# Kernel optimization log

Hardware: AMD Instinct MI355X
Metric: run time of the kernel (lower is better)

## Reference

```python
import jax, jax.numpy as jnp
import numpy as np


def fwht(x):
    """Unnormalized Fast Walsh-Hadamard transform along axis 0 (Sylvester order).
    Equivalent to H @ x where H is the +/-1 Hadamard matrix. x.shape[0] must be a power of 2."""
    D = x.shape[0]
    orig_shape = x.shape
    x = x.reshape(D, -1)
    h = 1
    while h < D:
        x = x.reshape(D // (2 * h), 2, h, -1)
        a = x[:, 0]
        b = x[:, 1]
        x = jnp.stack([a + b, a - b], axis=1)
        h *= 2
    return x.reshape(orig_shape)


def setup_inputs() -> dict:
    D = 4096
    B = 2048
    key = jax.random.key(0)
    k_x, k_eps, k_rho = jax.random.split(key, 3)
    x = jax.random.normal(k_x, (B, D), dtype=jnp.float32)
    epsilon = jax.random.normal(k_eps, (D,), dtype=jnp.float32)
    s1 = jnp.ones((D,), dtype=jnp.float32) * 0.01
    s2 = jnp.ones((D,), dtype=jnp.float32) * 0.01
    g_mu = jnp.zeros((D,), dtype=jnp.float32)
    # g_rho ~ Uniform(-5, -4) as in the torch init
    g_rho = jax.random.uniform(k_rho, (D,), dtype=jnp.float32, minval=-5.0, maxval=-4.0)
    return {"x": x, "epsilon": epsilon, "s1": s1, "s2": s2, "g_mu": g_mu, "g_rho": g_rho}


def reference(x, epsilon, s1, s2, g_mu, g_rho):
    D = s1.shape[0]
    # g_sigma_sqrt_diagonal = softplus(g_rho); sampled diag g = g_mu + sigma * eps.
    # W = diag(s1) @ H @ diag(g) @ H @ diag(s2); mu and sigma terms are linear in g, so combine.
    g = g_mu + jax.nn.softplus(g_rho) * epsilon
    # HS2 = H * s2 (columns of H scaled by s2) = H @ diag(s2) = fwht(diag(s2)) along axis 0
    HS2 = fwht(jnp.diag(s2))                      # [D, D]
    W = s1[:, None] * fwht(g[:, None] * HS2)      # [D, D]
    # F.linear(x, W) = x @ W^T
    return x @ W.T
```

## Files before the change

### kernel.cpp

```cpp
#include <hip/hip_runtime.h>
#include <math.h>

#define DIM 4096
#define ROWS 2048

__global__ void g_precompute(const float* __restrict__ eps,
                             const float* __restrict__ g_mu,
                             const float* __restrict__ g_rho,
                             float* __restrict__ g, int n) {
    int i = blockIdx.x * blockDim.x + threadIdx.x;
    if (i < n) {
        float sp = log1pf(expf(g_rho[i]));
        g[i] = g_mu[i] + sp * eps[i];
    }
}

__device__ __forceinline__ float4 f4mul(float4 a, float4 b) {
    return make_float4(a.x * b.x, a.y * b.y, a.z * b.z, a.w * b.w);
}

__device__ __forceinline__ void lane_stage(float4 v[16], int m, float sg) {
#pragma unroll
    for (int j = 0; j < 16; ++j) {
        float px = __shfl_xor(v[j].x, m, 64);
        float py = __shfl_xor(v[j].y, m, 64);
        float pz = __shfl_xor(v[j].z, m, 64);
        float pw = __shfl_xor(v[j].w, m, 64);
        v[j].x = fmaf(sg, v[j].x, px);
        v[j].y = fmaf(sg, v[j].y, py);
        v[j].z = fmaf(sg, v[j].z, pz);
        v[j].w = fmaf(sg, v[j].w, pw);
    }
}

__device__ __forceinline__ void fwht4096(float4 v[16], const float sg[6]) {
#pragma unroll
    for (int j = 0; j < 16; ++j) {
        float4 a = v[j];
        float t0 = a.x + a.y, t1 = a.x - a.y;
        float t2 = a.z + a.w, t3 = a.z - a.w;
        v[j] = make_float4(t0 + t2, t1 + t3, t0 - t2, t1 - t3);
    }
#pragma unroll
    for (int s = 0; s < 6; ++s)
        lane_stage(v, 1 << s, sg[s]);
#pragma unroll
    for (int m = 1; m < 16; m <<= 1) {
#pragma unroll
        for (int j = 0; j < 16; ++j) {
            if (!(j & m)) {
                int k = j | m;
                float4 a = v[j], b = v[k];
                v[j] = make_float4(a.x + b.x, a.y + b.y, a.z + b.z, a.w + b.w);
                v[k] = make_float4(a.x - b.x, a.y - b.y, a.z - b.z, a.w - b.w);
            }
        }
    }
}

__global__ void __launch_bounds__(256, 2)
whvi_main(const float* __restrict__ x, const float* __restrict__ s1,
          const float* __restrict__ s2, const float* __restrict__ g,
          float* __restrict__ out) {
    const int lane = threadIdx.x & 63;
    const int row  = blockIdx.x * 4 + (threadIdx.x >> 6);
    if (row >= ROWS) return;

    const float4* __restrict__ xr  = (const float4*)(x + (size_t)row * DIM);
    float4* __restrict__       orw = (float4*)(out + (size_t)row * DIM);
    const float4* __restrict__ s2v = (const float4*)s2;
    const float4* __restrict__ gv  = (const float4*)g;
    const float4* __restrict__ s1v = (const float4*)s1;

    float sg[6];
#pragma unroll
    for (int s = 0; s < 6; ++s)
        sg[s] = (lane & (1 << s)) ? -1.0f : 1.0f;

    float4 v[16];
#pragma unroll
    for (int j = 0; j < 16; ++j)
        v[j] = f4mul(xr[lane + 64 * j], s2v[lane + 64 * j]);

    fwht4096(v, sg);

#pragma unroll
    for (int j = 0; j < 16; ++j)
        v[j] = f4mul(v[j], gv[lane + 64 * j]);

    fwht4096(v, sg);

#pragma unroll
    for (int j = 0; j < 16; ++j)
        orw[lane + 64 * j] = f4mul(v[j], s1v[lane + 64 * j]);
}

extern "C" void kernel_launch(void* const* d_in, const int* in_sizes, int n_in,
                              void* d_out, int out_size, void* d_ws, size_t ws_size,
                              hipStream_t stream) {
    const float* x     = (const float*)d_in[0];
    const float* eps   = (const float*)d_in[1];
    const float* s1    = (const float*)d_in[2];
    const float* s2    = (const float*)d_in[3];
    const float* g_mu  = (const float*)d_in[4];
    const float* g_rho = (const float*)d_in[5];
    float* out = (float*)d_out;
    float* g   = (float*)d_ws;

    g_precompute<<<DIM / 256, 256, 0, stream>>>(eps, g_mu, g_rho, g, DIM);
    whvi_main<<<ROWS / 4, 256, 0, stream>>>(x, s1, s2, g, out);
}
```

Measured before the change: 107.0 us.

## Replace cross-lane shuffle FWHT stages with LDS transpose and in-register butterflies

Replaces the six __shfl_xor butterfly stages of each 4096-point FWHT with a padded LDS transpose, so the lane-dimension stages run as in-register butterflies on 64 values per thread. The two middle FWHT passes are merged around the g scaling, which needs only two transposes, and g is precomputed in a permuted layout to match. This cuts shuffle traffic (12 stages × 64 shuffles per thread) but adds LDS use of about 66KB per block and a 64-float register array, which may lower occupancy or cause spills. The launch-bounds minimum-blocks hint is dropped.

```diff
diff --git a/kernel.cpp b/kernel.cpp
--- a/kernel.cpp
+++ b/kernel.cpp
@@ -3,37 +3,24 @@
 
 #define DIM 4096
 #define ROWS 2048
+#define LSTR 65
 
 __global__ void g_precompute(const float* __restrict__ eps,
                              const float* __restrict__ g_mu,
                              const float* __restrict__ g_rho,
-                             float* __restrict__ g, int n) {
-    int i = blockIdx.x * blockDim.x + threadIdx.x;
-    if (i < n) {
-        float sp = log1pf(expf(g_rho[i]));
-        g[i] = g_mu[i] + sp * eps[i];
-    }
+                             float* __restrict__ g_t) {
+    int t = blockIdx.x * blockDim.x + threadIdx.x;
+    int lp = t >> 6, m = t & 63;
+    int j = 256 * (lp >> 2) + 4 * m + (lp & 3);
+    float sp = log1pf(expf(g_rho[j]));
+    g_t[t] = g_mu[j] + sp * eps[j];
 }
 
 __device__ __forceinline__ float4 f4mul(float4 a, float4 b) {
     return make_float4(a.x * b.x, a.y * b.y, a.z * b.z, a.w * b.w);
 }
 
-__device__ __forceinline__ void lane_stage(float4 v[16], int m, float sg) {
-#pragma unroll
-    for (int j = 0; j < 16; ++j) {
-        float px = __shfl_xor(v[j].x, m, 64);
-        float py = __shfl_xor(v[j].y, m, 64);
-        float pz = __shfl_xor(v[j].z, m, 64);
-        float pw = __shfl_xor(v[j].w, m, 64);
-        v[j].x = fmaf(sg, v[j].x, px);
-        v[j].y = fmaf(sg, v[j].y, py);
-        v[j].z = fmaf(sg, v[j].z, pz);
-        v[j].w = fmaf(sg, v[j].w, pw);
-    }
-}
-
-__device__ __forceinline__ void fwht4096(float4 v[16], const float sg[6]) {
+__device__ __forceinline__ void fwht_ri(float4 v[16]) {
 #pragma unroll
     for (int j = 0; j < 16; ++j) {
         float4 a = v[j];
@@ -41,9 +28,6 @@
         float t2 = a.z + a.w, t3 = a.z - a.w;
         v[j] = make_float4(t0 + t2, t1 + t3, t0 - t2, t1 - t3);
     }
-#pragma unroll
-    for (int s = 0; s < 6; ++s)
-        lane_stage(v, 1 << s, sg[s]);
 #pragma unroll
     for (int m = 1; m < 16; m <<= 1) {
 #pragma unroll
@@ -58,41 +42,87 @@
     }
 }
 
-__global__ void __launch_bounds__(256, 2)
+__device__ __forceinline__ void fwht_m(float f[64]) {
+#pragma unroll
+    for (int s = 0; s < 6; ++s) {
+        const int h = 1 << s;
+#pragma unroll
+        for (int m = 0; m < 64; ++m) {
+            if (!(m & h)) {
+                const int k = m | h;
+                float a = f[m], b = f[k];
+                f[m] = a + b;
+                f[k] = a - b;
+            }
+        }
+    }
+}
+
+__global__ void __launch_bounds__(256)
 whvi_main(const float* __restrict__ x, const float* __restrict__ s1,
-          const float* __restrict__ s2, const float* __restrict__ g,
+          const float* __restrict__ s2, const float* __restrict__ g_t,
           float* __restrict__ out) {
     const int lane = threadIdx.x & 63;
-    const int row  = blockIdx.x * 4 + (threadIdx.x >> 6);
-    if (row >= ROWS) return;
+    const int wid  = threadIdx.x >> 6;
+    const int row  = blockIdx.x * 4 + wid;
+
+    __shared__ float lds[4 * 64 * LSTR];
+    float* __restrict__ L = lds + wid * 64 * LSTR;
 
     const float4* __restrict__ xr  = (const float4*)(x + (size_t)row * DIM);
     float4* __restrict__       orw = (float4*)(out + (size_t)row * DIM);
     const float4* __restrict__ s2v = (const float4*)s2;
-    const float4* __restrict__ gv  = (const float4*)g;
     const float4* __restrict__ s1v = (const float4*)s1;
-
-    float sg[6];
-#pragma unroll
-    for (int s = 0; s < 6; ++s)
-        sg[s] = (lane & (1 << s)) ? -1.0f : 1.0f;
+    const float4* __restrict__ gtv = (const float4*)g_t;
 
     float4 v[16];
 #pragma unroll
-    for (int j = 0; j < 16; ++j)
-        v[j] = f4mul(xr[lane + 64 * j], s2v[lane + 64 * j]);
+    for (int r = 0; r < 16; ++r)
+        v[r] = f4mul(xr[64 * r + lane], s2v[64 * r + lane]);
 
-    fwht4096(v, sg);
+    fwht_ri(v);
 
 #pragma unroll
-    for (int j = 0; j < 16; ++j)
-        v[j] = f4mul(v[j], gv[lane + 64 * j]);
+    for (int r = 0; r < 16; ++r) {
+        L[lane * LSTR + 4 * r + 0] = v[r].x;
+        L[lane * LSTR + 4 * r + 1] = v[r].y;
+        L[lane * LSTR + 4 * r + 2] = v[r].z;
+        L[lane * LSTR + 4 * r + 3] = v[r].w;
+    }
+    float f[64];
+#pragma unroll
+    for (int m = 0; m < 64; ++m)
+        f[m] = L[m * LSTR + lane];
 
-    fwht4096(v, sg);
+    fwht_m(f);
 
 #pragma unroll
-    for (int j = 0; j < 16; ++j)
-        orw[lane + 64 * j] = f4mul(v[j], s1v[lane + 64 * j]);
+    for (int k = 0; k < 16; ++k) {
+        float4 gg = gtv[lane * 16 + k];
+        f[4 * k + 0] *= gg.x;
+        f[4 * k + 1] *= gg.y;
+        f[4 * k + 2] *= gg.z;
+        f[4 * k + 3] *= gg.w;
+    }
+
+    fwht_m(f);
+
+#pragma unroll
+    for (int m = 0; m < 64; ++m)
+        L[lane * LSTR + m] = f[m];
+#pragma unroll
+    for (int r = 0; r < 16; ++r) {
+        v[r].x = L[(4 * r + 0) * LSTR + lane];
+        v[r].y = L[(4 * r + 1) * LSTR + lane];
+        v[r].z = L[(4 * r + 2) * LSTR + lane];
+        v[r].w = L[(4 * r + 3) * LSTR + lane];
+    }
+
+    fwht_ri(v);
+
+#pragma unroll
+    for (int r = 0; r < 16; ++r)
+        orw[64 * r + lane] = f4mul(v[r], s1v[64 * r + lane]);
 }
 
 extern "C" void kernel_launch(void* const* d_in, const int* in_sizes, int n_in,
@@ -105,8 +135,8 @@
     const float* g_mu  = (const float*)d_in[4];
     const float* g_rho = (const float*)d_in[5];
     float* out = (float*)d_out;
-    float* g   = (float*)d_ws;
+    float* g_t = (float*)d_ws;
 
-    g_precompute<<<DIM / 256, 256, 0, stream>>>(eps, g_mu, g_rho, g, DIM);
-    whvi_main<<<ROWS / 4, 256, 0, stream>>>(x, s1, s2, g, out);
+    g_precompute<<<DIM / 256, 256, 0, stream>>>(eps, g_mu, g_rho, g_t);
+    whvi_main<<<ROWS / 4, 256, 0, stream>>>(x, s1, s2, g_t, out);
 }
```

Measured after the change: 100.9 us. 5.6% less time.

## Compute Walsh-Hadamard transforms with fp16 MFMA via 64x64 factorization in LDS

Applied to the files above, without the earlier changes.

Replaces the shuffle-based butterfly FWHT with a factorized H4096 = H64 ⊗ H64 applied as matrix multiplies on MFMA units. Each wave stages its row as a 64x64 fp16 tile in LDS, multiplies by a register-resident ±1 H64 fragment, and transposes through LDS between stages. This removes the many cross-lane shuffles. In exchange it adds LDS traffic and rounds intermediates to fp16, which may cost accuracy given the growth of values through the unnormalized transforms.

```diff
diff --git a/kernel.cpp b/kernel.cpp
--- a/kernel.cpp
+++ b/kernel.cpp
@@ -3,96 +3,132 @@
 
 #define DIM 4096
 #define ROWS 2048
+#define SB 68
+
+typedef _Float16 half8  __attribute__((ext_vector_type(8)));
+typedef _Float16 half4  __attribute__((ext_vector_type(4)));
+typedef float    float4e __attribute__((ext_vector_type(4)));
 
 __global__ void g_precompute(const float* __restrict__ eps,
                              const float* __restrict__ g_mu,
                              const float* __restrict__ g_rho,
-                             float* __restrict__ g, int n) {
+                             float* __restrict__ g) {
     int i = blockIdx.x * blockDim.x + threadIdx.x;
-    if (i < n) {
-        float sp = log1pf(expf(g_rho[i]));
-        g[i] = g_mu[i] + sp * eps[i];
-    }
+    g[i] = fmaf(log1pf(expf(g_rho[i])), eps[i], g_mu[i]);
 }
 
-__device__ __forceinline__ float4 f4mul(float4 a, float4 b) {
-    return make_float4(a.x * b.x, a.y * b.y, a.z * b.z, a.w * b.w);
+__device__ __forceinline__ void hx_stage(const _Float16* __restrict__ img,
+                                         int n, int q, const half8 Hf[4][2],
+                                         float4e acc[4][4]) {
+    half8 B[4][2];
+#pragma unroll
+    for (int J = 0; J < 4; ++J)
+#pragma unroll
+        for (int Kt = 0; Kt < 2; ++Kt) {
+            const _Float16* p = img + (32 * Kt + 8 * q) * SB + 16 * J + n;
+            half8 b;
+#pragma unroll
+            for (int j = 0; j < 8; ++j) b[j] = p[j * SB];
+            B[J][Kt] = b;
+        }
+#pragma unroll
+    for (int I = 0; I < 4; ++I)
+#pragma unroll
+        for (int J = 0; J < 4; ++J) {
+            float4e c = {0.0f, 0.0f, 0.0f, 0.0f};
+            c = __builtin_amdgcn_mfma_f32_16x16x32_f16(Hf[I][0], B[J][0], c, 0, 0, 0);
+            c = __builtin_amdgcn_mfma_f32_16x16x32_f16(Hf[I][1], B[J][1], c, 0, 0, 0);
+            acc[I][J] = c;
+        }
 }
 
-__device__ __forceinline__ void lane_stage(float4 v[16], int m, float sg) {
+__device__ __forceinline__ void img_write_T(_Float16* __restrict__ img,
+                                            int n, int q, const float4e acc[4][4]) {
 #pragma unroll
-    for (int j = 0; j < 16; ++j) {
-        float px = __shfl_xor(v[j].x, m, 64);
-        float py = __shfl_xor(v[j].y, m, 64);
-        float pz = __shfl_xor(v[j].z, m, 64);
-        float pw = __shfl_xor(v[j].w, m, 64);
-        v[j].x = fmaf(sg, v[j].x, px);
-        v[j].y = fmaf(sg, v[j].y, py);
-        v[j].z = fmaf(sg, v[j].z, pz);
-        v[j].w = fmaf(sg, v[j].w, pw);
-    }
-}
-
-__device__ __forceinline__ void fwht4096(float4 v[16], const float sg[6]) {
+    for (int I = 0; I < 4; ++I)
 #pragma unroll
-    for (int j = 0; j < 16; ++j) {
-        float4 a = v[j];
-        float t0 = a.x + a.y, t1 = a.x - a.y;
-        float t2 = a.z + a.w, t3 = a.z - a.w;
-        v[j] = make_float4(t0 + t2, t1 + t3, t0 - t2, t1 - t3);
-    }
-#pragma unroll
-    for (int s = 0; s < 6; ++s)
-        lane_stage(v, 1 << s, sg[s]);
-#pragma unroll
-    for (int m = 1; m < 16; m <<= 1) {
-#pragma unroll
-        for (int j = 0; j < 16; ++j) {
-            if (!(j & m)) {
-                int k = j | m;
-                float4 a = v[j], b = v[k];
-                v[j] = make_float4(a.x + b.x, a.y + b.y, a.z + b.z, a.w + b.w);
-                v[k] = make_float4(a.x - b.x, a.y - b.y, a.z - b.z, a.w - b.w);
-            }
+        for (int J = 0; J < 4; ++J) {
+            half4 h;
+            h[0] = (_Float16)acc[I][J][0];
+            h[1] = (_Float16)acc[I][J][1];
+            h[2] = (_Float16)acc[I][J][2];
+            h[3] = (_Float16)acc[I][J][3];
+            *(half4*)(img + (16 * J + n) * SB + 16 * I + 4 * q) = h;
         }
-    }
 }
 
 __global__ void __launch_bounds__(256, 2)
-whvi_main(const float* __restrict__ x, const float* __restrict__ s1,
+whvi_mfma(const float* __restrict__ x, const float* __restrict__ s1,
           const float* __restrict__ s2, const float* __restrict__ g,
           float* __restrict__ out) {
     const int lane = threadIdx.x & 63;
-    const int row  = blockIdx.x * 4 + (threadIdx.x >> 6);
-    if (row >= ROWS) return;
+    const int wid  = threadIdx.x >> 6;
+    const int row  = blockIdx.x * 4 + wid;
+    const int n = lane & 15, q = lane >> 4;
 
-    const float4* __restrict__ xr  = (const float4*)(x + (size_t)row * DIM);
-    float4* __restrict__       orw = (float4*)(out + (size_t)row * DIM);
-    const float4* __restrict__ s2v = (const float4*)s2;
-    const float4* __restrict__ gv  = (const float4*)g;
-    const float4* __restrict__ s1v = (const float4*)s1;
+    __shared__ __align__(16) _Float16 lds[4 * 64 * SB];
+    _Float16* __restrict__ img = lds + wid * 64 * SB;
 
-    float sg[6];
+    const float4e* __restrict__ xr  = (const float4e*)(x + (size_t)row * DIM);
+    const float4e* __restrict__ s2v = (const float4e*)s2;
+
+    float4e xv[16], sv[16];
 #pragma unroll
-    for (int s = 0; s < 6; ++s)
-        sg[s] = (lane & (1 << s)) ? -1.0f : 1.0f;
+    for (int r = 0; r < 16; ++r) xv[r] = xr[64 * r + lane];
+#pragma unroll
+    for (int r = 0; r < 16; ++r) sv[r] = s2v[64 * r + lane];
 
-    float4 v[16];
+    half8 Hf[4][2];
 #pragma unroll
-    for (int j = 0; j < 16; ++j)
-        v[j] = f4mul(xr[lane + 64 * j], s2v[lane + 64 * j]);
-
-    fwht4096(v, sg);
+    for (int I = 0; I < 4; ++I)
+#pragma unroll
+        for (int Kt = 0; Kt < 2; ++Kt) {
+            half8 h;
+#pragma unroll
+            for (int j = 0; j < 8; ++j) {
+                int rr = 16 * I + n, cc = 32 * Kt + 8 * q + j;
+                h[j] = (__popc(rr & cc) & 1) ? (_Float16)(-1.0f) : (_Float16)(1.0f);
+            }
+            Hf[I][Kt] = h;
+        }
 
 #pragma unroll
-    for (int j = 0; j < 16; ++j)
-        v[j] = f4mul(v[j], gv[lane + 64 * j]);
+    for (int r = 0; r < 16; ++r) {
+        float4e p = xv[r] * sv[r];
+        half4 h;
+        h[0] = (_Float16)p[0]; h[1] = (_Float16)p[1];
+        h[2] = (_Float16)p[2]; h[3] = (_Float16)p[3];
+        *(half4*)(img + (4 * r + q) * SB + 4 * n) = h;
+    }
 
-    fwht4096(v, sg);
+    float4e acc[4][4];
+
+    hx_stage(img, n, q, Hf, acc);
+    img_write_T(img, n, q, acc);
+    hx_stage(img, n, q, Hf, acc);
 
 #pragma unroll
-    for (int j = 0; j < 16; ++j)
-        orw[lane + 64 * j] = f4mul(v[j], s1v[lane + 64 * j]);
+    for (int I = 0; I < 4; ++I)
+#pragma unroll
+        for (int J = 0; J < 4; ++J) {
+            const float4e gg = *(const float4e*)(g + 1024 * J + 64 * n + 16 * I + 4 * q);
+            acc[I][J] *= gg;
+        }
+
+    img_write_T(img, n, q, acc);
+    hx_stage(img, n, q, Hf, acc);
+    img_write_T(img, n, q, acc);
+    hx_stage(img, n, q, Hf, acc);
+
+    float* __restrict__ orow = out + (size_t)row * DIM;
+#pragma unroll
+    for (int I = 0; I < 4; ++I)
+#pragma unroll
+        for (int J = 0; J < 4; ++J) {
+            const int e = 1024 * J + 64 * n + 16 * I + 4 * q;
+            const float4e sg = *(const float4e*)(s1 + e);
+            *(float4e*)(orow + e) = acc[I][J] * sg;
+        }
 }
 
 extern "C" void kernel_launch(void* const* d_in, const int* in_sizes, int n_in,
@@ -107,6 +143,6 @@
     float* out = (float*)d_out;
     float* g   = (float*)d_ws;
 
-    g_precompute<<<DIM / 256, 256, 0, stream>>>(eps, g_mu, g_rho, g, DIM);
-    whvi_main<<<ROWS / 4, 256, 0, stream>>>(x, s1, s2, g, out);
+    g_precompute<<<DIM / 256, 256, 0, stream>>>(eps, g_mu, g_rho, g);
+    whvi_mfma<<<ROWS / 4, 256, 0, stream>>>(x, s1, s2, g, out);
 }
```

New measurement: 100.2 us, median of 2. 1.07x faster.
